# Optimization experiments

Hardware: AMD Instinct MI355X
Metric: run time of the kernel (lower is better)

Reference implementation:

```python
import jax, jax.numpy as jnp
import numpy as np

C = 1.0          # Poincare ball curvature
H = 8            # num_heads
EPS = 1e-15
DELTA = 1e-7
SC = np.sqrt(C)  # sqrt curvature


def _norm(x):
    return jnp.sqrt(jnp.clip(jnp.sum(x * x, -1, keepdims=True), 1e-15))


def mobius_add(x, y):
    xy = jnp.sum(x * y, -1, keepdims=True)
    x2 = jnp.sum(x * x, -1, keepdims=True)
    y2 = jnp.sum(y * y, -1, keepdims=True)
    num = (1 + 2 * C * xy + C * y2) * x + (1 - C * x2) * y
    den = 1 + 2 * C * xy + C * C * x2 * y2
    return num / (den + EPS)


def mobius_matvec(W, x):
    xn = _norm(x)
    mx = x @ W.T
    mxn = _norm(mx)
    arg = jnp.clip(SC * xn, None, 1 - 1e-5)
    return jnp.tanh(mxn / xn * jnp.arctanh(arg)) * mx / (mxn * SC)


def logmap0(x):
    xn = _norm(x)
    return jnp.arctanh(jnp.clip(SC * xn, None, 1 - 1e-5)) * x / (SC * xn)


def expmap0(u):
    un = _norm(u)
    return jnp.tanh(SC * un) * u / (SC * un)


def hyp_linear(W, b, x):
    return mobius_add(mobius_matvec(W, x), b)


def setup_inputs() -> dict:
    key = jax.random.key(0)
    ks = jax.random.split(key, 5)
    B, S, E = 2, 512, 256
    x = jax.random.normal(ks[0], (B, S, E), jnp.float32) * 0.02  # inside unit ball
    scale = float(np.sqrt(6.0 / (E + E)))  # xavier uniform bound
    Wq = jax.random.uniform(ks[1], (E, E), jnp.float32, -scale, scale)
    Wk = jax.random.uniform(ks[2], (E, E), jnp.float32, -scale, scale)
    Wv = jax.random.uniform(ks[3], (E, E), jnp.float32, -scale, scale)
    Wo = jax.random.uniform(ks[4], (E, E), jnp.float32, -scale, scale)
    z = jnp.zeros((E,), jnp.float32)
    head_scaling = jnp.ones((H, 1, 1), jnp.float32)
    return {"x": x, "Wq": Wq, "bq": z, "Wk": Wk, "bk": z, "Wv": Wv, "bv": z,
            "Wo": Wo, "bo": z, "head_scaling": head_scaling}


def reference(x, Wq, bq, Wk, bk, Wv, bv, Wo, bo, head_scaling):
    B, S, E = x.shape
    D = E // H
    q = hyp_linear(Wq, bq, x).reshape(B, S, H, D).transpose(0, 2, 1, 3)  # (B,H,S,D)
    k = hyp_linear(Wk, bk, x).reshape(B, S, H, D).transpose(0, 2, 1, 3)
    v = hyp_linear(Wv, bv, x).reshape(B, S, H, D).transpose(0, 2, 1, 3)
    max_norm = (1 - 1e-5) / SC
    q = jnp.minimum(q, max_norm)  # elementwise clamp_max, faithful to source
    k = jnp.minimum(k, max_norm)
    qn = C * jnp.sum(q * q, -1)[..., :, None]   # (B,H,Sq,1)
    kn = C * jnp.sum(k * k, -1)[..., None, :]   # (B,H,1,Sk)
    # pairwise mobius_add(-k, q): (B,H,Sq,Sk,D)
    diff = mobius_add(-k[:, :, None, :, :], q[:, :, :, None, :])
    dn = C * jnp.sum(diff * diff, -1)           # (B,H,Sq,Sk)
    denom = (1 - qn) * (1 - kn) + EPS
    a = jnp.maximum(1 + 2 * dn / denom, 1 + DELTA)
    dist = jnp.log(a + jnp.sqrt(a * a - 1))     # acosh
    scores = -dist / (head_scaling * np.sqrt(D))
    w = jax.nn.softmax(scores, -1)
    out = expmap0(jnp.einsum('bhqk,bhkd->bhqd', w, logmap0(v)))
    out = out.transpose(0, 2, 1, 3).reshape(B, S, E)
    return hyp_linear(Wo, bo, out)
```

## Files before the change

kernel.cpp:

```cpp
#include <hip/hip_runtime.h>
#include <math.h>

#define Ec 256
#define Sc 512
#define Bc 2
#define Hc 8
#define Dc 32
#define MAXNORM (1.0f - 1e-5f)
#define NEc (Bc * Sc * Ec)
#define KSQ 2
#define KSO 4
#define NROWS (Bc * Hc * Sc)

__device__ __forceinline__ float fullWaveSum(float v) {
#pragma unroll
  for (int m = 32; m >= 1; m >>= 1) v += __shfl_xor(v, m, 64);
  return v;
}
__device__ __forceinline__ float halfWaveSum(float v) {
#pragma unroll
  for (int m = 16; m >= 1; m >>= 1) v += __shfl_xor(v, m, 64);
  return v;
}
__device__ __forceinline__ float atanh_fast(float z) {
  return 0.5f * __logf((1.0f + z) / (1.0f - z));
}
__device__ __forceinline__ float tanh_fast(float a) {
  float e = __expf(-2.0f * a);
  return (1.0f - e) / (1.0f + e);
}

__global__ __launch_bounds__(128) void gemm_xwt(
    const float* __restrict__ X,
    const float* __restrict__ W0, const float* __restrict__ W1,
    const float* __restrict__ W2,
    float* __restrict__ O0, float* __restrict__ O1, float* __restrict__ O2,
    const int nk) {
  const int tid = threadIdx.x;
  const int bx = blockIdx.x;
  const int by = blockIdx.y;
  const int kz = blockIdx.z;
  const int mat = by >> 2;
  const int cb0 = (by & 3) * 64;
  const int rb0 = bx * 32;
  const int kk0 = kz * 64 * nk;
  const float* __restrict__ W = (mat == 0) ? W0 : (mat == 1) ? W1 : W2;
  float* __restrict__ O = ((mat == 0) ? O0 : (mat == 1) ? O1 : O2) + (size_t)kz * NEc;

  __shared__ float Xs[64][36];
  __shared__ float Ws[64][68];

  const int f4 = tid & 15;
  const int sub = tid >> 4;
  const int ty = tid >> 4;
  const int tx = tid & 15;

  float acc[4][4];
#pragma unroll
  for (int i = 0; i < 4; ++i)
#pragma unroll
    for (int j = 0; j < 4; ++j) acc[i][j] = 0.f;

  for (int c = 0; c < nk; ++c) {
    const int kk = kk0 + c * 64;
    __syncthreads();
#pragma unroll
    for (int i = 0; i < 4; ++i) {
      int row = sub + i * 8;
      float4 v = *(const float4*)&X[(size_t)(rb0 + row) * Ec + kk + f4 * 4];
      Xs[f4 * 4 + 0][row] = v.x;
      Xs[f4 * 4 + 1][row] = v.y;
      Xs[f4 * 4 + 2][row] = v.z;
      Xs[f4 * 4 + 3][row] = v.w;
    }
#pragma unroll
    for (int i = 0; i < 8; ++i) {
      int col = sub + i * 8;
      float4 v = *(const float4*)&W[(size_t)(cb0 + col) * Ec + kk + f4 * 4];
      Ws[f4 * 4 + 0][col] = v.x;
      Ws[f4 * 4 + 1][col] = v.y;
      Ws[f4 * 4 + 2][col] = v.z;
      Ws[f4 * 4 + 3][col] = v.w;
    }
    __syncthreads();
#pragma unroll 8
    for (int k = 0; k < 64; ++k) {
      float4 a = *(const float4*)&Xs[k][ty * 4];
      float4 b = *(const float4*)&Ws[k][tx * 4];
      float av[4] = {a.x, a.y, a.z, a.w};
      float bv[4] = {b.x, b.y, b.z, b.w};
#pragma unroll
      for (int i = 0; i < 4; ++i)
#pragma unroll
        for (int j = 0; j < 4; ++j) acc[i][j] = fmaf(av[i], bv[j], acc[i][j]);
    }
  }
#pragma unroll
  for (int i = 0; i < 4; ++i) {
    float4 o = make_float4(acc[i][0], acc[i][1], acc[i][2], acc[i][3]);
    *(float4*)&O[(size_t)(rb0 + ty * 4 + i) * Ec + cb0 + tx * 4] = o;
  }
}

__global__ __launch_bounds__(256) void qkv_stats(
    const float* __restrict__ x,
    const float* __restrict__ mxq, const float* __restrict__ mxk,
    const float* __restrict__ mxv,
    const float* __restrict__ bq, const float* __restrict__ bk,
    const float* __restrict__ bv,
    float* __restrict__ qo, float* __restrict__ ko, float* __restrict__ lvo,
    float* __restrict__ qno, float* __restrict__ kno) {
  const int t = threadIdx.x;
  const int row = blockIdx.x;
  const int b = row >> 9;
  const int s = row & (Sc - 1);
  const size_t idx = (size_t)row * Ec + t;
  const float xv = x[idx];
  float mq = 0.f, mk = 0.f, mv = 0.f;
#pragma unroll
  for (int p = 0; p < KSQ; ++p) {
    mq += mxq[idx + (size_t)p * NEc];
    mk += mxk[idx + (size_t)p * NEc];
    mv += mxv[idx + (size_t)p * NEc];
  }
  const float bb[3] = {bq[t], bk[t], bv[t]};
  const float mvals[3] = {mq, mk, mv};

  float vals[10] = {xv * xv,
                    mq * mq, mq * bb[0], bb[0] * bb[0],
                    mk * mk, mk * bb[1], bb[1] * bb[1],
                    mv * mv, mv * bb[2], bb[2] * bb[2]};
  __shared__ float red[10][4];
  __shared__ float fin[10];
#pragma unroll
  for (int i = 0; i < 10; ++i) {
    float v = fullWaveSum(vals[i]);
    if ((t & 63) == 0) red[i][t >> 6] = v;
  }
  __syncthreads();
  if (t < 10) fin[t] = red[t][0] + red[t][1] + red[t][2] + red[t][3];
  __syncthreads();

  const float x2 = fin[0];
  const float xn = sqrtf(fmaxf(x2, 1e-15f));
  const float at = atanh_fast(fminf(xn, MAXNORM));
  const int h = t >> 5;

#pragma unroll
  for (int m = 0; m < 3; ++m) {
    float mx2 = fin[1 + 3 * m];
    float mxb = fin[2 + 3 * m];
    float b2 = fin[3 + 3 * m];
    float mxn = sqrtf(fmaxf(mx2, 1e-15f));
    float scl = tanh_fast((mxn / xn) * at) / mxn;
    float mvv = scl * mvals[m];
    float X2 = scl * scl * mx2;
    float XY = scl * mxb;
    float numc = 1.0f + 2.0f * XY + b2;
    float den = 1.0f + 2.0f * XY + X2 * b2 + 1e-15f;
    float res = (numc * mvv + (1.0f - X2) * bb[m]) / den;
    if (m < 2) {
      res = fminf(res, MAXNORM);
      float s2 = halfWaveSum(res * res);
      if (m == 0) {
        qo[idx] = res;
        if ((t & 31) == 0) qno[(b * Hc + h) * Sc + s] = s2;
      } else {
        ko[idx] = res;
        if ((t & 31) == 0) kno[(b * Hc + h) * Sc + s] = s2;
      }
    } else {
      float vn2 = halfWaveSum(res * res);
      float vn = sqrtf(fmaxf(vn2, 1e-15f));
      float f = atanh_fast(fminf(vn, MAXNORM)) / vn;
      lvo[idx] = f * res;
    }
  }
}

__global__ __launch_bounds__(256) void attn_fused(
    const float* __restrict__ q, const float* __restrict__ k,
    const float* __restrict__ lv, const float* __restrict__ qn,
    const float* __restrict__ kn, const float* __restrict__ hs,
    float* __restrict__ out) {
  const int tid = threadIdx.x;
  const int sq0 = blockIdx.x * 16;
  const int bh = blockIdx.y;
  const int b = bh >> 3;
  const int h = bh & 7;

  __shared__ float Qst[Dc][17];
  __shared__ float Kst[Dc][68];
  __shared__ float LVs[2][64][36];
  __shared__ float Pst[64][17];
  __shared__ float knS[64];
  __shared__ float redD[4][16];
  __shared__ float redN[4][16];

  const int r = tid & 15;
  const int c4 = tid >> 4;

  if (tid < 128) {
    int qr = tid >> 3, dq = tid & 7;
    float4 v = *(const float4*)&q[(size_t)(b * Sc + sq0 + qr) * Ec + h * Dc + dq * 4];
    Qst[dq * 4 + 0][qr] = v.x;
    Qst[dq * 4 + 1][qr] = v.y;
    Qst[dq * 4 + 2][qr] = v.z;
    Qst[dq * 4 + 3][qr] = v.w;
  }
  const float q2 = qn[bh * Sc + sq0 + r];
  const float omq = 1.0f - q2;
  const float sinv = -1.0f / (hs[h] * sqrtf((float)Dc));

  float out0 = 0.f, out1 = 0.f, den_acc = 0.f;

  const int srow = tid >> 3;
  const int sdq = tid & 7;

  for (int t = 0; t < 8; ++t) {
    const int j0 = t * 64;
    const int buf = t & 1;
#pragma unroll
    for (int i = 0; i < 2; ++i) {
      int row = srow + i * 32;
      const size_t gidx = (size_t)(b * Sc + j0 + row) * Ec + h * Dc + sdq * 4;
      float4 kv = *(const float4*)&k[gidx];
      Kst[sdq * 4 + 0][row] = kv.x;
      Kst[sdq * 4 + 1][row] = kv.y;
      Kst[sdq * 4 + 2][row] = kv.z;
      Kst[sdq * 4 + 3][row] = kv.w;
      float4 lvv = *(const float4*)&lv[gidx];
      *(float4*)&LVs[buf][row][sdq * 4] = lvv;
    }
    if (tid < 64) knS[tid] = kn[bh * Sc + j0 + tid];
    __syncthreads();

    float p[4] = {0.f, 0.f, 0.f, 0.f};
#pragma unroll
    for (int kk = 0; kk < Dc; ++kk) {
      float qv = Qst[kk][r];
      float4 kvv = *(const float4*)&Kst[kk][c4 * 4];
      p[0] = fmaf(qv, kvv.x, p[0]);
      p[1] = fmaf(qv, kvv.y, p[1]);
      p[2] = fmaf(qv, kvv.z, p[2]);
      p[3] = fmaf(qv, kvv.w, p[3]);
    }
    float4 k2v = *(const float4*)&knS[c4 * 4];
    float kk2[4] = {k2v.x, k2v.y, k2v.z, k2v.w};
    float ps = 0.f;
#pragma unroll
    for (int j = 0; j < 4; ++j) {
      const float k2 = kk2[j];
      const float kq = p[j];
      const float omk = 1.0f - k2;
      float s2x2 = fmaf(-4.0f, kq, 2.0f * k2 + 2.0f * q2);
      float dden = fmaf(k2, q2, fmaf(-2.0f, kq, 1.0f)) + 1e-15f;
      float Pd = fmaf(dden, omk * omq, 1e-20f);
      float rp = __builtin_amdgcn_rcpf(Pd);
      float tt = fmaxf(s2x2 * rp, 1e-7f);
      float z = (1.0f + tt) + sqrtf(fmaf(tt, tt, tt + tt));
      float po = __builtin_amdgcn_exp2f(sinv * __builtin_amdgcn_logf(z));
      Pst[c4 * 4 + j][r] = po;
      ps += po;
    }
    den_acc += ps;
    __syncthreads();

#pragma unroll 8
    for (int j = 0; j < 64; ++j) {
      float pj = Pst[j][r];
      float2 l2 = *(const float2*)&LVs[buf][j][c4 * 2];
      out0 = fmaf(pj, l2.x, out0);
      out1 = fmaf(pj, l2.y, out1);
    }
  }

  float d = den_acc;
  d += __shfl_xor(d, 16, 64);
  d += __shfl_xor(d, 32, 64);
  const int wv = tid >> 6;
  if ((tid & 63) < 16) redD[wv][r] = d;
  __syncthreads();
  const float den = redD[0][r] + redD[1][r] + redD[2][r] + redD[3][r];
  const float li = 1.0f / den;
  float o0 = out0 * li, o1 = out1 * li;

  float un2 = fmaf(o0, o0, o1 * o1);
  un2 += __shfl_xor(un2, 16, 64);
  un2 += __shfl_xor(un2, 32, 64);
  if ((tid & 63) < 16) redN[wv][r] = un2;
  __syncthreads();
  un2 = redN[0][r] + redN[1][r] + redN[2][r] + redN[3][r];
  float un = sqrtf(fmaxf(un2, 1e-15f));
  float f = tanh_fast(un) / un;
  float2 ov = make_float2(o0 * f, o1 * f);
  *(float2*)&out[(size_t)(b * Sc + sq0 + r) * Ec + h * Dc + c4 * 2] = ov;
}

__global__ __launch_bounds__(256) void proj_stats(
    const float* __restrict__ xin, const float* __restrict__ mx,
    const float* __restrict__ bo, float* __restrict__ out) {
  const int t = threadIdx.x;
  const int row = blockIdx.x;
  const size_t idx = (size_t)row * Ec + t;
  const float xv = xin[idx];
  float m = 0.f;
#pragma unroll
  for (int p = 0; p < KSO; ++p) m += mx[idx + (size_t)p * NEc];
  const float bb = bo[t];
  float vals[4] = {xv * xv, m * m, m * bb, bb * bb};
  __shared__ float red[4][4];
  __shared__ float fin[4];
#pragma unroll
  for (int i = 0; i < 4; ++i) {
    float v = fullWaveSum(vals[i]);
    if ((t & 63) == 0) red[i][t >> 6] = v;
  }
  __syncthreads();
  if (t < 4) fin[t] = red[t][0] + red[t][1] + red[t][2] + red[t][3];
  __syncthreads();

  float x2 = fin[0], mx2 = fin[1], mxb = fin[2], b2 = fin[3];
  float xn = sqrtf(fmaxf(x2, 1e-15f));
  float mxn = sqrtf(fmaxf(mx2, 1e-15f));
  float scl = tanh_fast((mxn / xn) * atanh_fast(fminf(xn, MAXNORM))) / mxn;
  float mvv = scl * m;
  float X2 = scl * scl * mx2;
  float XY = scl * mxb;
  float numc = 1.0f + 2.0f * XY + b2;
  float den = 1.0f + 2.0f * XY + X2 * b2 + 1e-15f;
  out[idx] = (numc * mvv + (1.0f - X2) * bb) / den;
}

extern "C" void kernel_launch(void* const* d_in, const int* in_sizes, int n_in,
                              void* d_out, int out_size, void* d_ws, size_t ws_size,
                              hipStream_t stream) {
  (void)in_sizes; (void)n_in; (void)out_size; (void)ws_size;
  const float* x  = (const float*)d_in[0];
  const float* Wq = (const float*)d_in[1];
  const float* bq = (const float*)d_in[2];
  const float* Wk = (const float*)d_in[3];
  const float* bk = (const float*)d_in[4];
  const float* Wv = (const float*)d_in[5];
  const float* bv = (const float*)d_in[6];
  const float* Wo = (const float*)d_in[7];
  const float* bo = (const float*)d_in[8];
  const float* hs = (const float*)d_in[9];

  float* ws = (float*)d_ws;
  const int NE = NEc;
  const int NH = NROWS;
  float* mxq = ws;
  float* mxk = mxq + KSQ * NE;
  float* mxv = mxk + KSQ * NE;
  float* mxo = mxv + KSQ * NE;
  float* qb  = mxo + KSO * NE;
  float* kb  = qb + NE;
  float* lvb = kb + NE;
  float* aob = lvb + NE;
  float* qnb = aob + NE;
  float* knb = qnb + NH;

  const int M = Bc * Sc;

  gemm_xwt<<<dim3(M / 32, 12, KSQ), 128, 0, stream>>>(x, Wq, Wk, Wv,
                                                      mxq, mxk, mxv, 2);
  qkv_stats<<<M, 256, 0, stream>>>(x, mxq, mxk, mxv, bq, bk, bv,
                                   qb, kb, lvb, qnb, knb);
  attn_fused<<<dim3(32, 16), 256, 0, stream>>>(qb, kb, lvb, qnb, knb, hs, aob);
  gemm_xwt<<<dim3(M / 32, 4, KSO), 128, 0, stream>>>(aob, Wo, Wo, Wo,
                                                     mxo, mxo, mxo, 1);
  proj_stats<<<M, 256, 0, stream>>>(aob, mxo, bo, (float*)d_out);
}
```

Baseline: 133.8 us.

## Register-block attention and enlarge GEMM tiles for more reuse per thread

Attention now processes 32 queries per block with 128-key tiles, and each thread computes a 4x4 score block and a 4x8 PV accumulator held in registers. Q is cached in registers and the partial PV sums are reduced across threads through a shared-memory union. The GEMM tile grows from 32x64 to 64x64 with a 4x8 accumulator per thread. This raises arithmetic per shared-memory load, but it halves the block counts (256 attention blocks, fewer GEMM blocks) and increases register pressure, so occupancy may drop.

Result: no change. 132.9 us (-0.6%).

```diff
diff --git a/kernel.cpp b/kernel.cpp
--- a/kernel.cpp
+++ b/kernel.cpp
@@ -11,6 +11,8 @@
 #define KSQ 2
 #define KSO 4
 #define NROWS (Bc * Hc * Sc)
+#define KT 128
+#define NT (Sc / KT)
 
 __device__ __forceinline__ float fullWaveSum(float v) {
 #pragma unroll
@@ -42,63 +44,62 @@
   const int kz = blockIdx.z;
   const int mat = by >> 2;
   const int cb0 = (by & 3) * 64;
-  const int rb0 = bx * 32;
+  const int rb0 = bx * 64;
   const int kk0 = kz * 64 * nk;
   const float* __restrict__ W = (mat == 0) ? W0 : (mat == 1) ? W1 : W2;
   float* __restrict__ O = ((mat == 0) ? O0 : (mat == 1) ? O1 : O2) + (size_t)kz * NEc;
 
-  __shared__ float Xs[64][36];
+  __shared__ float Xs[64][68];
   __shared__ float Ws[64][68];
 
   const int f4 = tid & 15;
   const int sub = tid >> 4;
-  const int ty = tid >> 4;
-  const int tx = tid & 15;
-
-  float acc[4][4];
+  const int r4 = tid >> 3;
+  const int c8 = tid & 7;
+
+  float acc[4][8];
 #pragma unroll
   for (int i = 0; i < 4; ++i)
 #pragma unroll
-    for (int j = 0; j < 4; ++j) acc[i][j] = 0.f;
+    for (int j = 0; j < 8; ++j) acc[i][j] = 0.f;
 
   for (int c = 0; c < nk; ++c) {
     const int kk = kk0 + c * 64;
     __syncthreads();
 #pragma unroll
-    for (int i = 0; i < 4; ++i) {
+    for (int i = 0; i < 8; ++i) {
       int row = sub + i * 8;
       float4 v = *(const float4*)&X[(size_t)(rb0 + row) * Ec + kk + f4 * 4];
       Xs[f4 * 4 + 0][row] = v.x;
       Xs[f4 * 4 + 1][row] = v.y;
       Xs[f4 * 4 + 2][row] = v.z;
       Xs[f4 * 4 + 3][row] = v.w;
-    }
-#pragma unroll
-    for (int i = 0; i < 8; ++i) {
-      int col = sub + i * 8;
-      float4 v = *(const float4*)&W[(size_t)(cb0 + col) * Ec + kk + f4 * 4];
-      Ws[f4 * 4 + 0][col] = v.x;
-      Ws[f4 * 4 + 1][col] = v.y;
-      Ws[f4 * 4 + 2][col] = v.z;
-      Ws[f4 * 4 + 3][col] = v.w;
+      float4 w = *(const float4*)&W[(size_t)(cb0 + row) * Ec + kk + f4 * 4];
+      Ws[f4 * 4 + 0][row] = w.x;
+      Ws[f4 * 4 + 1][row] = w.y;
+      Ws[f4 * 4 + 2][row] = w.z;
+      Ws[f4 * 4 + 3][row] = w.w;
     }
     __syncthreads();
 #pragma unroll 8
     for (int k = 0; k < 64; ++k) {
-      float4 a = *(const float4*)&Xs[k][ty * 4];
-      float4 b = *(const float4*)&Ws[k][tx * 4];
+      float4 a = *(const float4*)&Xs[k][r4 * 4];
+      float4 b0 = *(const float4*)&Ws[k][c8 * 8];
+      float4 b1 = *(const float4*)&Ws[k][c8 * 8 + 4];
       float av[4] = {a.x, a.y, a.z, a.w};
-      float bv[4] = {b.x, b.y, b.z, b.w};
+      float bv[8] = {b0.x, b0.y, b0.z, b0.w, b1.x, b1.y, b1.z, b1.w};
 #pragma unroll
       for (int i = 0; i < 4; ++i)
 #pragma unroll
-        for (int j = 0; j < 4; ++j) acc[i][j] = fmaf(av[i], bv[j], acc[i][j]);
+        for (int j = 0; j < 8; ++j) acc[i][j] = fmaf(av[i], bv[j], acc[i][j]);
     }
   }
 #pragma unroll
   for (int i = 0; i < 4; ++i) {
-    float4 o = make_float4(acc[i][0], acc[i][1], acc[i][2], acc[i][3]);
-    *(float4*)&O[(size_t)(rb0 + ty * 4 + i) * Ec + cb0 + tx * 4] = o;
+    float4 o0 = make_float4(acc[i][0], acc[i][1], acc[i][2], acc[i][3]);
+    float4 o1 = make_float4(acc[i][4], acc[i][5], acc[i][6], acc[i][7]);
+    *(float4*)&O[(size_t)(rb0 + r4 * 4 + i) * Ec + cb0 + c8 * 8] = o0;
+    *(float4*)&O[(size_t)(rb0 + r4 * 4 + i) * Ec + cb0 + c8 * 8 + 4] = o1;
   }
 }
 
@@ -184,117 +185,223 @@
     const float* __restrict__ kn, const float* __restrict__ hs,
     float* __restrict__ out) {
   const int tid = threadIdx.x;
-  const int sq0 = blockIdx.x * 16;
+  const int sq0 = blockIdx.x * 32;
   const int bh = blockIdx.y;
   const int b = bh >> 3;
   const int h = bh & 7;
 
-  __shared__ float Qst[Dc][17];
-  __shared__ float Kst[Dc][68];
-  __shared__ float LVs[2][64][36];
-  __shared__ float Pst[64][17];
-  __shared__ float knS[64];
-  __shared__ float redD[4][16];
-  __shared__ float redN[4][16];
-
-  const int r = tid & 15;
-  const int c4 = tid >> 4;
-
-  if (tid < 128) {
-    int qr = tid >> 3, dq = tid & 7;
-    float4 v = *(const float4*)&q[(size_t)(b * Sc + sq0 + qr) * Ec + h * Dc + dq * 4];
-    Qst[dq * 4 + 0][qr] = v.x;
-    Qst[dq * 4 + 1][qr] = v.y;
-    Qst[dq * 4 + 2][qr] = v.z;
-    Qst[dq * 4 + 3][qr] = v.w;
-  }
-  const float q2 = qn[bh * Sc + sq0 + r];
-  const float omq = 1.0f - q2;
+  __shared__ float Qst[32][36];
+  __shared__ float LVs[128][36];
+  __shared__ float knS[128];
+  union SMU {
+    struct { float Kst[32][132]; float Pst[32][132]; } a;
+    struct { float accm[32 * 260]; } m;
+  };
+  __shared__ __align__(16) SMU u;
+
+  const int r4 = tid >> 5;
+  const int c4 = tid & 31;
+  const int dgrp = (tid >> 3) & 3;
+  const int jsl = tid & 7;
+  const int rr = tid >> 1;
+  const int half = tid & 1;
+
+  {
+    int qr = tid >> 3, dqq = tid & 7;
+    *(float4*)&Qst[qr][dqq * 4] =
+        *(const float4*)&q[(size_t)(b * Sc + sq0 + qr) * Ec + h * Dc + dqq * 4];
+  }
+  __syncthreads();
+  float4 qv0[8], qv1[8], qv2[8], qv3[8];
+#pragma unroll
+  for (int fd = 0; fd < 8; ++fd) {
+    qv0[fd] = *(const float4*)&Qst[r4 * 4 + 0][fd * 4];
+    qv1[fd] = *(const float4*)&Qst[r4 * 4 + 1][fd * 4];
+    qv2[fd] = *(const float4*)&Qst[r4 * 4 + 2][fd * 4];
+    qv3[fd] = *(const float4*)&Qst[r4 * 4 + 3][fd * 4];
+  }
+  float q2r[4], omq[4];
+#pragma unroll
+  for (int i = 0; i < 4; ++i) {
+    q2r[i] = qn[bh * Sc + sq0 + r4 * 4 + i];
+    omq[i] = 1.0f - q2r[i];
+  }
   const float sinv = -1.0f / (hs[h] * sqrtf((float)Dc));
 
-  float out0 = 0.f, out1 = 0.f, den_acc = 0.f;
-
-  const int srow = tid >> 3;
-  const int sdq = tid & 7;
-
-  for (int t = 0; t < 8; ++t) {
-    const int j0 = t * 64;
-    const int buf = t & 1;
-#pragma unroll
-    for (int i = 0; i < 2; ++i) {
-      int row = srow + i * 32;
-      const size_t gidx = (size_t)(b * Sc + j0 + row) * Ec + h * Dc + sdq * 4;
-      float4 kv = *(const float4*)&k[gidx];
-      Kst[sdq * 4 + 0][row] = kv.x;
-      Kst[sdq * 4 + 1][row] = kv.y;
-      Kst[sdq * 4 + 2][row] = kv.z;
-      Kst[sdq * 4 + 3][row] = kv.w;
-      float4 lvv = *(const float4*)&lv[gidx];
-      *(float4*)&LVs[buf][row][sdq * 4] = lvv;
-    }
-    if (tid < 64) knS[tid] = kn[bh * Sc + j0 + tid];
+  float4 acc0[4], acc1[4];
+#pragma unroll
+  for (int i = 0; i < 4; ++i) {
+    acc0[i] = make_float4(0.f, 0.f, 0.f, 0.f);
+    acc1[i] = make_float4(0.f, 0.f, 0.f, 0.f);
+  }
+  float dprt[4] = {0.f, 0.f, 0.f, 0.f};
+
+  for (int t = 0; t < NT; ++t) {
+    const int j0g = t * KT;
     __syncthreads();
-
-    float p[4] = {0.f, 0.f, 0.f, 0.f};
-#pragma unroll
-    for (int kk = 0; kk < Dc; ++kk) {
-      float qv = Qst[kk][r];
-      float4 kvv = *(const float4*)&Kst[kk][c4 * 4];
-      p[0] = fmaf(qv, kvv.x, p[0]);
-      p[1] = fmaf(qv, kvv.y, p[1]);
-      p[2] = fmaf(qv, kvv.z, p[2]);
-      p[3] = fmaf(qv, kvv.w, p[3]);
-    }
+    {
+      const size_t gbase = (size_t)(b * Sc + j0g + rr) * Ec + h * Dc;
+#pragma unroll
+      for (int i2 = 0; i2 < 4; ++i2) {
+        const int dqq = half * 4 + i2;
+        float4 kv = *(const float4*)&k[gbase + dqq * 4];
+        u.a.Kst[dqq * 4 + 0][rr] = kv.x;
+        u.a.Kst[dqq * 4 + 1][rr] = kv.y;
+        u.a.Kst[dqq * 4 + 2][rr] = kv.z;
+        u.a.Kst[dqq * 4 + 3][rr] = kv.w;
+        *(float4*)&LVs[rr][dqq * 4] = *(const float4*)&lv[gbase + dqq * 4];
+      }
+      if (tid < 128) knS[tid] = kn[bh * Sc + j0g + tid];
+    }
+    __syncthreads();
+
+    float p0[4] = {0.f, 0.f, 0.f, 0.f};
+    float p1[4] = {0.f, 0.f, 0.f, 0.f};
+    float p2[4] = {0.f, 0.f, 0.f, 0.f};
+    float p3[4] = {0.f, 0.f, 0.f, 0.f};
+#pragma unroll
+    for (int fd = 0; fd < 8; ++fd) {
+      float4 k0 = *(const float4*)&u.a.Kst[fd * 4 + 0][c4 * 4];
+      float4 k1 = *(const float4*)&u.a.Kst[fd * 4 + 1][c4 * 4];
+      float4 k2 = *(const float4*)&u.a.Kst[fd * 4 + 2][c4 * 4];
+      float4 k3 = *(const float4*)&u.a.Kst[fd * 4 + 3][c4 * 4];
+#define QKROW(A, P)                                                   \
+      P[0] = fmaf(A.x, k0.x, P[0]); P[0] = fmaf(A.y, k1.x, P[0]);     \
+      P[0] = fmaf(A.z, k2.x, P[0]); P[0] = fmaf(A.w, k3.x, P[0]);     \
+      P[1] = fmaf(A.x, k0.y, P[1]); P[1] = fmaf(A.y, k1.y, P[1]);     \
+      P[1] = fmaf(A.z, k2.y, P[1]); P[1] = fmaf(A.w, k3.y, P[1]);     \
+      P[2] = fmaf(A.x, k0.z, P[2]); P[2] = fmaf(A.y, k1.z, P[2]);     \
+      P[2] = fmaf(A.z, k2.z, P[2]); P[2] = fmaf(A.w, k3.z, P[2]);     \
+      P[3] = fmaf(A.x, k0.w, P[3]); P[3] = fmaf(A.y, k1.w, P[3]);     \
+      P[3] = fmaf(A.z, k2.w, P[3]); P[3] = fmaf(A.w, k3.w, P[3]);
+      { float4 a = qv0[fd]; QKROW(a, p0) }
+      { float4 a = qv1[fd]; QKROW(a, p1) }
+      { float4 a = qv2[fd]; QKROW(a, p2) }
+      { float4 a = qv3[fd]; QKROW(a, p3) }
+#undef QKROW
+    }
+
     float4 k2v = *(const float4*)&knS[c4 * 4];
-    float kk2[4] = {k2v.x, k2v.y, k2v.z, k2v.w};
-    float ps = 0.f;
-#pragma unroll
-    for (int j = 0; j < 4; ++j) {
-      const float k2 = kk2[j];
-      const float kq = p[j];
-      const float omk = 1.0f - k2;
-      float s2x2 = fmaf(-4.0f, kq, 2.0f * k2 + 2.0f * q2);
-      float dden = fmaf(k2, q2, fmaf(-2.0f, kq, 1.0f)) + 1e-15f;
-      float Pd = fmaf(dden, omk * omq, 1e-20f);
-      float rp = __builtin_amdgcn_rcpf(Pd);
-      float tt = fmaxf(s2x2 * rp, 1e-7f);
-      float z = (1.0f + tt) + sqrtf(fmaf(tt, tt, tt + tt));
-      float po = __builtin_amdgcn_exp2f(sinv * __builtin_amdgcn_logf(z));
-      Pst[c4 * 4 + j][r] = po;
-      ps += po;
-    }
-    den_acc += ps;
+    const float kk2[4] = {k2v.x, k2v.y, k2v.z, k2v.w};
+#define EPIROW(P, RIDX)                                                     \
+    {                                                                       \
+      float po[4];                                                          \
+      _Pragma("unroll")                                                     \
+      for (int j = 0; j < 4; ++j) {                                         \
+        const float k2 = kk2[j];                                            \
+        const float kq = P[j];                                              \
+        const float omk = 1.0f - k2;                                        \
+        float s2x2 = fmaf(-4.0f, kq, 2.0f * k2 + 2.0f * q2r[RIDX]);         \
+        float dden = fmaf(k2, q2r[RIDX], fmaf(-2.0f, kq, 1.0f)) + 1e-15f;   \
+        float Pd = fmaf(dden, omk * omq[RIDX], 1e-20f);                     \
+        float rp = __builtin_amdgcn_rcpf(Pd);                               \
+        float tt = fmaxf(s2x2 * rp, 1e-7f);                                 \
+        float z = (1.0f + tt) + sqrtf(fmaf(tt, tt, tt + tt));               \
+        po[j] = __builtin_amdgcn_exp2f(sinv * __builtin_amdgcn_logf(z));    \
+      }                                                                     \
+      dprt[RIDX] += (po[0] + po[1]) + (po[2] + po[3]);                      \
+      *(float4*)&u.a.Pst[r4 * 4 + RIDX][c4 * 4] =                           \
+          make_float4(po[0], po[1], po[2], po[3]);                          \
+    }
+    EPIROW(p0, 0)
+    EPIROW(p1, 1)
+    EPIROW(p2, 2)
+    EPIROW(p3, 3)
+#undef EPIROW
     __syncthreads();
 
-#pragma unroll 8
-    for (int j = 0; j < 64; ++j) {
-      float pj = Pst[j][r];
-      float2 l2 = *(const float2*)&LVs[buf][j][c4 * 2];
-      out0 = fmaf(pj, l2.x, out0);
-      out1 = fmaf(pj, l2.y, out1);
-    }
-  }
-
-  float d = den_acc;
-  d += __shfl_xor(d, 16, 64);
-  d += __shfl_xor(d, 32, 64);
-  const int wv = tid >> 6;
-  if ((tid & 63) < 16) redD[wv][r] = d;
-  __syncthreads();
-  const float den = redD[0][r] + redD[1][r] + redD[2][r] + redD[3][r];
-  const float li = 1.0f / den;
-  float o0 = out0 * li, o1 = out1 * li;
-
-  float un2 = fmaf(o0, o0, o1 * o1);
-  un2 += __shfl_xor(un2, 16, 64);
-  un2 += __shfl_xor(un2, 32, 64);
-  if ((tid & 63) < 16) redN[wv][r] = un2;
-  __syncthreads();
-  un2 = redN[0][r] + redN[1][r] + redN[2][r] + redN[3][r];
+#pragma unroll
+    for (int ch = 0; ch < 4; ++ch) {
+      const int j0 = ch * 32 + jsl * 4;
+      float4 pr0 = *(const float4*)&u.a.Pst[r4 * 4 + 0][j0];
+      float4 pr1 = *(const float4*)&u.a.Pst[r4 * 4 + 1][j0];
+      float4 pr2 = *(const float4*)&u.a.Pst[r4 * 4 + 2][j0];
+      float4 pr3 = *(const float4*)&u.a.Pst[r4 * 4 + 3][j0];
+      float4 la0 = *(const float4*)&LVs[j0 + 0][dgrp * 8];
+      float4 lb0 = *(const float4*)&LVs[j0 + 0][dgrp * 8 + 4];
+      float4 la1 = *(const float4*)&LVs[j0 + 1][dgrp * 8];
+      float4 lb1 = *(const float4*)&LVs[j0 + 1][dgrp * 8 + 4];
+      float4 la2 = *(const float4*)&LVs[j0 + 2][dgrp * 8];
+      float4 lb2 = *(const float4*)&LVs[j0 + 2][dgrp * 8 + 4];
+      float4 la3 = *(const float4*)&LVs[j0 + 3][dgrp * 8];
+      float4 lb3 = *(const float4*)&LVs[j0 + 3][dgrp * 8 + 4];
+#define PVROW(PR, I)                                                    \
+      acc0[I].x = fmaf(PR.x, la0.x, acc0[I].x);                         \
+      acc0[I].y = fmaf(PR.x, la0.y, acc0[I].y);                         \
+      acc0[I].z = fmaf(PR.x, la0.z, acc0[I].z);                         \
+      acc0[I].w = fmaf(PR.x, la0.w, acc0[I].w);                         \
+      acc1[I].x = fmaf(PR.x, lb0.x, acc1[I].x);                         \
+      acc1[I].y = fmaf(PR.x, lb0.y, acc1[I].y);                         \
+      acc1[I].z = fmaf(PR.x, lb0.z, acc1[I].z);                         \
+      acc1[I].w = fmaf(PR.x, lb0.w, acc1[I].w);                         \
+      acc0[I].x = fmaf(PR.y, la1.x, acc0[I].x);                         \
+      acc0[I].y = fmaf(PR.y, la1.y, acc0[I].y);                         \
+      acc0[I].z = fmaf(PR.y, la1.z, acc0[I].z);                         \
+      acc0[I].w = fmaf(PR.y, la1.w, acc0[I].w);                         \
+      acc1[I].x = fmaf(PR.y, lb1.x, acc1[I].x);                         \
+      acc1[I].y = fmaf(PR.y, lb1.y, acc1[I].y);                         \
+      acc1[I].z = fmaf(PR.y, lb1.z, acc1[I].z);                         \
+      acc1[I].w = fmaf(PR.y, lb1.w, acc1[I].w);                         \
+      acc0[I].x = fmaf(PR.z, la2.x, acc0[I].x);                         \
+      acc0[I].y = fmaf(PR.z, la2.y, acc0[I].y);                         \
+      acc0[I].z = fmaf(PR.z, la2.z, acc0[I].z);                         \
+      acc0[I].w = fmaf(PR.z, la2.w, acc0[I].w);                         \
+      acc1[I].x = fmaf(PR.z, lb2.x, acc1[I].x);                         \
+      acc1[I].y = fmaf(PR.z, lb2.y, acc1[I].y);                         \
+      acc1[I].z = fmaf(PR.z, lb2.z, acc1[I].z);                         \
+      acc1[I].w = fmaf(PR.z, lb2.w, acc1[I].w);                         \
+      acc0[I].x = fmaf(PR.w, la3.x, acc0[I].x);                         \
+      acc0[I].y = fmaf(PR.w, la3.y, acc0[I].y);                         \
+      acc0[I].z = fmaf(PR.w, la3.z, acc0[I].z);                         \
+      acc0[I].w = fmaf(PR.w, la3.w, acc0[I].w);                         \
+      acc1[I].x = fmaf(PR.w, lb3.x, acc1[I].x);                         \
+      acc1[I].y = fmaf(PR.w, lb3.y, acc1[I].y);                         \
+      acc1[I].z = fmaf(PR.w, lb3.z, acc1[I].z);                         \
+      acc1[I].w = fmaf(PR.w, lb3.w, acc1[I].w);
+      PVROW(pr0, 0)
+      PVROW(pr1, 1)
+      PVROW(pr2, 2)
+      PVROW(pr3, 3)
+#undef PVROW
+    }
+  }
+
+  __syncthreads();
+#pragma unroll
+  for (int i = 0; i < 4; ++i) {
+    *(float4*)&u.m.accm[(r4 * 4 + i) * 260 + jsl * 32 + dgrp * 8] = acc0[i];
+    *(float4*)&u.m.accm[(r4 * 4 + i) * 260 + jsl * 32 + dgrp * 8 + 4] = acc1[i];
+  }
+  float ds0 = halfWaveSum(dprt[0]);
+  float ds1 = halfWaveSum(dprt[1]);
+  float ds2 = halfWaveSum(dprt[2]);
+  float ds3 = halfWaveSum(dprt[3]);
+  if (c4 == 0) {
+    knS[r4 * 4 + 0] = ds0;
+    knS[r4 * 4 + 1] = ds1;
+    knS[r4 * 4 + 2] = ds2;
+    knS[r4 * 4 + 3] = ds3;
+  }
+  __syncthreads();
+
+  const int row = tid >> 3;
+  const int dseg = tid & 7;
+  float4 o = make_float4(0.f, 0.f, 0.f, 0.f);
+#pragma unroll
+  for (int g = 0; g < 8; ++g) {
+    float4 a = *(const float4*)&u.m.accm[row * 260 + g * 32 + dseg * 4];
+    o.x += a.x; o.y += a.y; o.z += a.z; o.w += a.w;
+  }
+  const float li = 1.0f / knS[row];
+  o.x *= li; o.y *= li; o.z *= li; o.w *= li;
+  float un2 = fmaf(o.x, o.x, fmaf(o.y, o.y, fmaf(o.z, o.z, o.w * o.w)));
+  un2 += __shfl_xor(un2, 4, 64);
+  un2 += __shfl_xor(un2, 2, 64);
+  un2 += __shfl_xor(un2, 1, 64);
   float un = sqrtf(fmaxf(un2, 1e-15f));
   float f = tanh_fast(un) / un;
-  float2 ov = make_float2(o0 * f, o1 * f);
-  *(float2*)&out[(size_t)(b * Sc + sq0 + r) * Ec + h * Dc + c4 * 2] = ov;
+  o.x *= f; o.y *= f; o.z *= f; o.w *= f;
+  *(float4*)&out[(size_t)(b * Sc + sq0 + row) * Ec + h * Dc + dseg * 4] = o;
 }
 
 __global__ __launch_bounds__(256) void proj_stats(
@@ -363,12 +470,12 @@
 
   const int M = Bc * Sc;
 
-  gemm_xwt<<<dim3(M / 32, 12, KSQ), 128, 0, stream>>>(x, Wq, Wk, Wv,
+  gemm_xwt<<<dim3(M / 64, 12, KSQ), 128, 0, stream>>>(x, Wq, Wk, Wv,
                                                       mxq, mxk, mxv, 2);
   qkv_stats<<<M, 256, 0, stream>>>(x, mxq, mxk, mxv, bq, bk, bv,
                                    qb, kb, lvb, qnb, knb);
-  attn_fused<<<dim3(32, 16), 256, 0, stream>>>(qb, kb, lvb, qnb, knb, hs, aob);
-  gemm_xwt<<<dim3(M / 32, 4, KSO), 128, 0, stream>>>(aob, Wo, Wo, Wo,
+  attn_fused<<<dim3(16, 16), 256, 0, stream>>>(qb, kb, lvb, qnb, knb, hs, aob);
+  gemm_xwt<<<dim3(M / 64, 4, KSO), 128, 0, stream>>>(aob, Wo, Wo, Wo,
                                                      mxo, mxo, mxo, 1);
   proj_stats<<<M, 256, 0, stream>>>(aob, mxo, bo, (float*)d_out);
 }
```
